# Kernel tuning notes

Measured on AMD Instinct MI355X. Metric: run time of the kernel, lower is better.

## Reference

```python
import jax, jax.numpy as jnp
import numpy as np

B, T, NH, HS = 2, 2048, 16, 64
C = NH * HS
V_SHIFT = 1          # value shift; queries start at position V_SHIFT
EXP_SCALE = 10.0     # exp_param_scale
KB_UP = 5.0          # kernel_beta_upbound


def setup_inputs() -> dict:
    key = jax.random.key(0)
    ks = jax.random.split(key, 8)
    s = 0.02
    return {
        "x": jax.random.normal(ks[0], (B, T, C), jnp.float32),
        # leaky-average key path: linear proj + per-head decay coefficient
        "W_la": jax.random.normal(ks[1], (C, C), jnp.float32) * s,
        "la_coef": jax.random.uniform(ks[2], (NH,), jnp.float32, 0.1, 0.9),
        "kernel_beta": jnp.ones((NH,), jnp.float32) / EXP_SCALE,
        "value_beta": jnp.ones((NH,), jnp.float32) * (-0.5) / EXP_SCALE,
        # value featurizer (lowrlinearconv): linear + per-head mixing coef
        "W_v": jax.random.normal(ks[3], (C, C), jnp.float32) * s,
        "v_coef": jax.random.uniform(ks[4], (NH,), jnp.float32, 0.0, 1.0),
        "W_proj": jax.random.normal(ks[5], (C, C), jnp.float32) * s,
    }


def reference(x, W_la, la_coef, kernel_beta, value_beta, W_v, v_coef, W_proj):
    B_, T_, C_ = x.shape
    # ---- keys: leaky average (per-head EMA recurrence) of linear projection ----
    xl = (x @ W_la).reshape(B_, T_, NH, HS)          # (B,T,nh,hs)
    alpha = la_coef.reshape(NH, 1)                   # per-head decay

    def step(carry, xt):  # carry,xt: (B,nh,hs)
        new = alpha * carry + (1.0 - alpha) * xt
        return new, new

    _, kt = jax.lax.scan(step, jnp.zeros((B_, NH, HS), x.dtype),
                         jnp.swapaxes(xl, 0, 1))    # (T,B,nh,hs)
    k = jnp.transpose(kt, (1, 2, 0, 3))              # (B,nh,T,hs)
    k = k / jnp.linalg.norm(k, axis=-1, keepdims=True)
    kb = jnp.exp(jnp.minimum(kernel_beta * EXP_SCALE, KB_UP)).reshape(1, NH, 1, 1)
    k = k * kb

    # ---- values: lowrlinearconv featurizer (shift=1, kernel=2) + L2 norm ----
    xv = (x @ W_v).reshape(B_, T_, NH, HS).transpose(0, 2, 1, 3)   # (B,nh,T,hs)
    xv_sh = jnp.concatenate([xv[:, :, 1:], jnp.zeros_like(xv[:, :, :1])], axis=2)
    c = v_coef.reshape(1, NH, 1, 1)
    v = xv_sh * (1.0 - c) + xv * c
    v = v / jnp.linalg.norm(v, axis=-1, keepdims=True)
    v = v * jnp.exp(value_beta * EXP_SCALE).reshape(1, NH, 1, 1)

    # ---- shifted-causal masked SDPA (scale=1); queries are positions >= V_SHIFT ----
    q = k[:, :, V_SHIFT:]                            # (B,nh,T-1,hs)
    scores = jnp.einsum('bhqd,bhkd->bhqk', q, k)
    qpos = jnp.arange(V_SHIFT, T_)[:, None]
    kpos = jnp.arange(T_)[None, :]
    mask = kpos < qpos                               # key j visible iff j < query position
    scores = jnp.where(mask, scores, -jnp.inf)
    att = jax.nn.softmax(scores, axis=-1)
    y_att = jnp.einsum('bhqk,bhkd->bhqd', att, v)
    y = jnp.concatenate([jnp.zeros((B_, NH, V_SHIFT, HS), x.dtype), y_att], axis=2)
    y = jnp.transpose(y, (0, 2, 1, 3)).reshape(B_, T_, C_)
    return y @ W_proj                                # dropouts are eval-mode identity
```

## Files before the change

### kernel.cpp

```cpp
#include <hip/hip_runtime.h>
#include <hip/hip_bf16.h>

#define B_  2
#define T_  2048
#define NH_ 16
#define HS_ 64
#define C_  1024
#define SCL_ 128
#define SCN_ (T_ / SCL_)
#define NT_  (T_ / 64)
#define TEL_ 4096

typedef __attribute__((ext_vector_type(8))) short bf16x8;
typedef __attribute__((ext_vector_type(4))) float f32x4;

__device__ inline int pack_bf16(float a, float b) {
  union { __hip_bfloat16 h; unsigned short u; } ua, ub;
  ua.h = __float2bfloat16(a);
  ub.h = __float2bfloat16(b);
  return (int)(((unsigned)ub.u << 16) | (unsigned)ua.u);
}

__device__ inline void gl_lds16(const __hip_bfloat16* g, __hip_bfloat16* l) {
  __builtin_amdgcn_global_load_lds(
      (const __attribute__((address_space(1))) unsigned int*)g,
      (__attribute__((address_space(3))) unsigned int*)l, 16, 0, 0);
}

__global__ __launch_bounds__(256) void prep1_kernel(const float* __restrict__ x,
                                                    const float* __restrict__ W_la,
                                                    const float* __restrict__ W_v,
                                                    const float* __restrict__ W_proj,
                                                    __hip_bfloat16* __restrict__ x16,
                                                    __hip_bfloat16* __restrict__ Wcat,
                                                    __hip_bfloat16* __restrict__ WprojT) {
  __shared__ __hip_bfloat16 tile[64][66];
  const int bid = (int)blockIdx.x;
  if (bid < 2048) {
    const int i = (bid * 256 + (int)threadIdx.x) * 8;
    const float4 a = *reinterpret_cast<const float4*>(x + i);
    const float4 b = *reinterpret_cast<const float4*>(x + i + 4);
    union { int s[4]; int4 v; } u;
    u.s[0] = pack_bf16(a.x, a.y);
    u.s[1] = pack_bf16(a.z, a.w);
    u.s[2] = pack_bf16(b.x, b.y);
    u.s[3] = pack_bf16(b.z, b.w);
    *reinterpret_cast<int4*>(x16 + i) = u.v;
    return;
  }
  const int id = bid - 2048;
  const int z = id >> 8;
  const int rem = id & 255;
  const int bx = rem & 15, by = rem >> 4;
  const float* W = (z == 0) ? W_la : (z == 1) ? W_v : W_proj;
  __hip_bfloat16* WT = (z == 2) ? WprojT : Wcat + (size_t)z * C_ * C_;
  const int w = threadIdx.x >> 6, l = threadIdx.x & 63;
  const int n0 = bx * 64, k0 = by * 64;
#pragma unroll
  for (int r = 0; r < 16; ++r) {
    const int k = k0 + w * 16 + r;
    tile[w * 16 + r][l] = __float2bfloat16(W[(size_t)k * C_ + n0 + l]);
  }
  __syncthreads();
#pragma unroll
  for (int r = 0; r < 16; ++r) {
    const int nn = w * 16 + r;
    WT[(size_t)(n0 + nn) * C_ + k0 + l] = tile[l][nn];
  }
}

__global__ __launch_bounds__(256) void gemm_in_kernel(const __hip_bfloat16* __restrict__ A,
                                                      const __hip_bfloat16* __restrict__ BT,
                                                      float* __restrict__ C0,
                                                      float* __restrict__ C1) {
  __shared__ __hip_bfloat16 As[2 * 128 * 32];
  __shared__ __hip_bfloat16 Bs[2 * 128 * 32];
  const int tid = threadIdx.x;
  const int m0 = blockIdx.y * 128, n0 = blockIdx.x * 128;
  const int w = tid >> 6, l = tid & 63;
  const int n = l & 15, kg = l >> 4;
  const int m0w = (w & 1) * 64, n0w = (w >> 1) * 64;

  const int r0 = tid >> 2, o0 = (tid & 3) * 8;
  const __hip_bfloat16* ag0 = A + (size_t)(m0 + r0) * C_ + o0;
  const __hip_bfloat16* ag1 = A + (size_t)(m0 + 64 + r0) * C_ + o0;
  const __hip_bfloat16* bg0 = BT + (size_t)(n0 + r0) * C_ + o0;
  const __hip_bfloat16* bg1 = BT + (size_t)(n0 + 64 + r0) * C_ + o0;

  f32x4 acc[4][4];
#pragma unroll
  for (int i = 0; i < 4; ++i)
#pragma unroll
    for (int j = 0; j < 4; ++j) acc[i][j] = f32x4{0.f, 0.f, 0.f, 0.f};

  auto stage = [&](int kk, int buf) {
    __hip_bfloat16* a = As + buf * 4096;
    __hip_bfloat16* b = Bs + buf * 4096;
    gl_lds16(ag0 + kk, a + tid * 8);
    gl_lds16(ag1 + kk, a + 2048 + tid * 8);
    gl_lds16(bg0 + kk, b + tid * 8);
    gl_lds16(bg1 + kk, b + 2048 + tid * 8);
  };

  stage(0, 0);
  int cur = 0;
  for (int k0 = 0; k0 < C_; k0 += 32) {
    asm volatile("" ::: "memory");
    __builtin_amdgcn_s_barrier();
    asm volatile("" ::: "memory");
    if (k0 + 32 < C_) {
      stage(k0 + 32, cur ^ 1);
      asm volatile("s_waitcnt vmcnt(4)" ::: "memory");
    } else {
      asm volatile("s_waitcnt vmcnt(0)" ::: "memory");
    }
    __builtin_amdgcn_s_barrier();
    asm volatile("" ::: "memory");

    const __hip_bfloat16* Ab = As + cur * 4096;
    const __hip_bfloat16* Bb = Bs + cur * 4096;
    bf16x8 af[4], bf[4];
#pragma unroll
    for (int ms = 0; ms < 4; ++ms)
      af[ms] = *reinterpret_cast<const bf16x8*>(Ab + (m0w + ms * 16 + n) * 32 + kg * 8);
#pragma unroll
    for (int ns = 0; ns < 4; ++ns)
      bf[ns] = *reinterpret_cast<const bf16x8*>(Bb + (n0w + ns * 16 + n) * 32 + kg * 8);
#pragma unroll
    for (int ms = 0; ms < 4; ++ms)
#pragma unroll
      for (int ns = 0; ns < 4; ++ns)
        acc[ms][ns] = __builtin_amdgcn_mfma_f32_16x16x32_bf16(af[ms], bf[ns], acc[ms][ns], 0, 0, 0);
    cur ^= 1;
  }

  float* Cb = (n0 < C_) ? C0 : C1;
  const int nc = (n0 < C_) ? n0 : n0 - C_;
#pragma unroll
  for (int ms = 0; ms < 4; ++ms) {
#pragma unroll
    for (int r = 0; r < 4; ++r) {
      const int row = m0 + m0w + ms * 16 + kg * 4 + r;
      float* cp = Cb + (size_t)row * C_ + nc + n0w + n;
#pragma unroll
      for (int ns = 0; ns < 4; ++ns) cp[ns * 16] = acc[ms][ns][r];
    }
  }
}

__global__ __launch_bounds__(256) void gemm_proj_kernel(const __hip_bfloat16* __restrict__ A,
                                                        const __hip_bfloat16* __restrict__ BT,
                                                        float* __restrict__ Cout) {
  __shared__ __hip_bfloat16 As[2 * 64 * 32];
  __shared__ __hip_bfloat16 Bs[2 * 128 * 32];
  const int tid = threadIdx.x;
  const int m0 = blockIdx.y * 64, n0 = blockIdx.x * 128;
  const int w = tid >> 6, l = tid & 63;
  const int n = l & 15, kg = l >> 4;

  const int r0 = tid >> 2, o0 = (tid & 3) * 8;
  const __hip_bfloat16* ag = A + (size_t)(m0 + r0) * C_ + o0;
  const __hip_bfloat16* bg0 = BT + (size_t)(n0 + r0) * C_ + o0;
  const __hip_bfloat16* bg1 = BT + (size_t)(n0 + 64 + r0) * C_ + o0;

  f32x4 acc[4][2];
#pragma unroll
  for (int i = 0; i < 4; ++i)
#pragma unroll
    for (int j = 0; j < 2; ++j) acc[i][j] = f32x4{0.f, 0.f, 0.f, 0.f};

  auto stage = [&](int kk, int buf) {
    __hip_bfloat16* a = As + buf * 2048;
    __hip_bfloat16* b = Bs + buf * 4096;
    gl_lds16(ag + kk, a + tid * 8);
    gl_lds16(bg0 + kk, b + tid * 8);
    gl_lds16(bg1 + kk, b + 2048 + tid * 8);
  };

  stage(0, 0);
  int cur = 0;
  for (int k0 = 0; k0 < C_; k0 += 32) {
    asm volatile("" ::: "memory");
    __builtin_amdgcn_s_barrier();
    asm volatile("" ::: "memory");
    if (k0 + 32 < C_) {
      stage(k0 + 32, cur ^ 1);
      asm volatile("s_waitcnt vmcnt(3)" ::: "memory");
    } else {
      asm volatile("s_waitcnt vmcnt(0)" ::: "memory");
    }
    __builtin_amdgcn_s_barrier();
    asm volatile("" ::: "memory");

    const __hip_bfloat16* Ab = As + cur * 2048;
    const __hip_bfloat16* Bb = Bs + cur * 4096;
    bf16x8 af[4], bf[2];
#pragma unroll
    for (int ms = 0; ms < 4; ++ms)
      af[ms] = *reinterpret_cast<const bf16x8*>(Ab + (ms * 16 + n) * 32 + kg * 8);
#pragma unroll
    for (int ns = 0; ns < 2; ++ns)
      bf[ns] = *reinterpret_cast<const bf16x8*>(Bb + (w * 32 + ns * 16 + n) * 32 + kg * 8);
#pragma unroll
    for (int ms = 0; ms < 4; ++ms)
#pragma unroll
      for (int ns = 0; ns < 2; ++ns)
        acc[ms][ns] = __builtin_amdgcn_mfma_f32_16x16x32_bf16(af[ms], bf[ns], acc[ms][ns], 0, 0, 0);
    cur ^= 1;
  }

#pragma unroll
  for (int ms = 0; ms < 4; ++ms) {
#pragma unroll
    for (int r = 0; r < 4; ++r) {
      const int row = m0 + ms * 16 + kg * 4 + r;
      float* cp = Cout + (size_t)row * C_ + n0 + w * 32 + n;
#pragma unroll
      for (int ns = 0; ns < 2; ++ns) cp[ns * 16] = acc[ms][ns][r];
    }
  }
}

__global__ __launch_bounds__(256) void prep2_kernel(const float* __restrict__ xv,
                                                    const float* __restrict__ xl,
                                                    __hip_bfloat16* __restrict__ vt,
                                                    float* __restrict__ loc,
                                                    float* __restrict__ carr,
                                                    const float* __restrict__ value_beta,
                                                    const float* __restrict__ v_coef,
                                                    const float* __restrict__ la_coef) {
  __shared__ float4 smem4[2048];
  const int bid = (int)blockIdx.x;
  if (bid < 1024) {
    __hip_bfloat16 (*tile)[66] = reinterpret_cast<__hip_bfloat16(*)[66]>(smem4);
    const int tc = bid % NT_;
    const int bh = bid / NT_;
    const int h = bh % NH_, b = bh / NH_;
    const int t0 = tc * 64;
    const int w = threadIdx.x >> 6, l = threadIdx.x & 63;

    const float c = v_coef[h];
    const float vb = expf(value_beta[h] * 10.0f);

    for (int r = 0; r < 16; ++r) {
      const int tl = w * 16 + r;
      const int t = t0 + tl;
      const float* base = xv + ((size_t)b * T_ + t) * C_ + h * HS_ + l;
      const float cu = base[0];
      const float nxt = (t + 1 < T_) ? base[C_] : 0.0f;
      float val = nxt * (1.0f - c) + cu * c;
      float ssum = val * val;
#pragma unroll
      for (int m = 32; m; m >>= 1) ssum += __shfl_xor(ssum, m);
      tile[tl][l] = __float2bfloat16(val * (vb / sqrtf(ssum)));
    }
    __syncthreads();
    __hip_bfloat16* vtb = vt + (size_t)(bh * NT_ + tc) * TEL_;
    const int kk = l >> 3, j = l & 7;
    for (int rr = 0; rr < 16; ++rr) {
      const int hs = w * 16 + rr;
      vtb[(kk * 64 + hs) * 8 + j] = tile[l][hs];
    }
    return;
  }
  {
    float* buf = reinterpret_cast<float*>(smem4);
    const int idx = bid - 1024;
    const int c = idx % SCN_;
    const int bh = idx / SCN_;
    const int b = bh / NH_, h = bh % NH_;
    const int tid = threadIdx.x;
    const int t0 = c * SCL_;

    const float alpha = la_coef[h];
    const float onema = 1.0f - alpha;
    const float4* src4 = reinterpret_cast<const float4*>(xl + (size_t)b * T_ * C_ + h * HS_);

    float4* buf4 = reinterpret_cast<float4*>(buf);
#pragma unroll
    for (int i = 0; i < (SCL_ * HS_ / 4) / 256; ++i) {
      const int ix = tid + i * 256;
      const int tt = ix >> 4, d4 = ix & 15;
      buf4[tt * 16 + d4] = src4[(size_t)(t0 + tt) * (C_ / 4) + d4];
    }
    __syncthreads();
    if (tid < 64) {
      const int d = tid;
      float c2 = 0.0f;
#pragma unroll 8
      for (int tt = 0; tt < SCL_; ++tt) {
        c2 = alpha * c2 + onema * buf[tt * HS_ + d];
        buf[tt * HS_ + d] = c2;
      }
      carr[(size_t)(bh * SCN_ + c) * HS_ + d] = c2;
    }
    __syncthreads();
    float4* dst4 = reinterpret_cast<float4*>(loc + ((size_t)bh * T_ + t0) * HS_);
#pragma unroll
    for (int i = 0; i < (SCL_ * HS_ / 4) / 256; ++i) dst4[tid + i * 256] = buf4[tid + i * 256];
  }
}

__global__ __launch_bounds__(256) void ema_fix_norm_kernel(const float* __restrict__ loc,
                                                           const float* __restrict__ carr,
                                                           __hip_bfloat16* __restrict__ kb16,
                                                           const float* __restrict__ la_coef,
                                                           const float* __restrict__ kernel_beta) {
  const int c = blockIdx.x % SCN_;
  const int bh = blockIdx.x / SCN_;
  const int h = bh % NH_;
  const int w = threadIdx.x >> 6, l = threadIdx.x & 63;

  const float alpha = la_coef[h];
  const float aL = __powf(alpha, (float)SCL_);
  const float kbs = expf(fminf(kernel_beta[h] * 10.0f, 5.0f));

  float A = 0.0f;
  for (int cc = 0; cc < c; ++cc) A = aL * A + carr[(size_t)(bh * SCN_ + cc) * HS_ + l];

  const float* lp = loc + ((size_t)bh * T_ + c * SCL_ + w * 32) * HS_ + l;
  __hip_bfloat16* kt = kb16 + (size_t)bh * NT_ * TEL_;
  const int g = l >> 3, j = l & 7;

  float s = __powf(alpha, (float)(w * 32 + 1));
  for (int rr = 0; rr < 32; ++rr) {
    const int t = c * SCL_ + w * 32 + rr;
    float val = lp[rr * HS_] + s * A;
    float ss = val * val;
#pragma unroll
    for (int m = 32; m; m >>= 1) ss += __shfl_xor(ss, m);
    const int tile = t >> 6, key = t & 63;
    kt[(size_t)tile * TEL_ + (g * 64 + key) * 8 + j] = __float2bfloat16(val * (kbs / sqrtf(ss)));
    s *= alpha;
  }
}

__global__ __launch_bounds__(256, 4) void attn_mfma_kernel(
    const __hip_bfloat16* __restrict__ kb,
    const __hip_bfloat16* __restrict__ vt,
    __hip_bfloat16* __restrict__ y) {
  __shared__ __hip_bfloat16 Ks[2][2 * TEL_];
  __shared__ __hip_bfloat16 Ps[4][16 * 64];

  const int id = (int)blockIdx.x;
  const int xcd = id & 7;
  const int s = id >> 3;
  const int bh = xcd + 8 * (s & 3);
  const int v = s >> 2;
  const int qt = (v < 16) ? (31 - v) : (v - 16);
  const int b = bh / NH_, h = bh % NH_;
  const int q0 = qt * 64;
  const int w = threadIdx.x >> 6;
  const int l = threadIdx.x & 63;
  const int n = l & 15;
  const int kg = l >> 4;
  const int qq = w * 16 + n;
  const int query = q0 + qq;
  const int lo = l * 8;
  const int tb = bh * NT_;
  const int so = w * 1024 + lo;

  bf16x8 qf0, qf1;
  {
    const __hip_bfloat16* qtile = kb + (size_t)(tb + qt) * TEL_;
    qf0 = *reinterpret_cast<const bf16x8*>(qtile + (kg * 64 + qq) * 8);
    qf1 = *reinterpret_cast<const bf16x8*>(qtile + ((kg + 4) * 64 + qq) * 8);
  }
  const __hip_bfloat16* vbase = vt + (size_t)tb * TEL_ + (kg * 64 + n) * 8;

  f32x4 accO[4];
#pragma unroll
  for (int i = 0; i < 4; ++i) accO[i] = f32x4{0.f, 0.f, 0.f, 0.f};
  float l_acc = 0.0f;

  __hip_bfloat16* Pw = Ps[w];
  int* Pwi = reinterpret_cast<int*>(Pw);

  auto stage2 = [&](int j0, int buf) {
    const size_t tg = (size_t)(tb + j0) * TEL_;
    __hip_bfloat16* Kb = &Ks[buf][0];
    gl_lds16(kb + tg + so, Kb + so);
    gl_lds16(kb + tg + so + 512, Kb + so + 512);
    gl_lds16(kb + tg + TEL_ + so, Kb + TEL_ + so);
    gl_lds16(kb + tg + TEL_ + so + 512, Kb + TEL_ + so + 512);
  };
  auto stage1 = [&](int j0, int buf) {
    const size_t tg = (size_t)(tb + j0) * TEL_;
    __hip_bfloat16* Kb = &Ks[buf][0];
    gl_lds16(kb + tg + so, Kb + so);
    gl_lds16(kb + tg + so + 512, Kb + so + 512);
  };
  auto loadV = [&](int jt, bf16x8 (&vf)[2][4]) {
    const __hip_bfloat16* vp = vbase + (size_t)jt * TEL_;
#pragma unroll
    for (int ks = 0; ks < 2; ++ks)
#pragma unroll
      for (int mo = 0; mo < 4; ++mo)
        vf[ks][mo] = *reinterpret_cast<const bf16x8*>(vp + ks * 2048 + mo * 128);
  };
  auto computeS = [&](const __hip_bfloat16* Kc, f32x4 (&accS)[4]) {
    __builtin_amdgcn_s_setprio(1);
#pragma unroll
    for (int ms = 0; ms < 4; ++ms) {
      bf16x8 a0 = *reinterpret_cast<const bf16x8*>(Kc + (kg * 64 + ms * 16 + n) * 8);
      bf16x8 a1 = *reinterpret_cast<const bf16x8*>(Kc + ((kg + 4) * 64 + ms * 16 + n) * 8);
      f32x4 z{0.f, 0.f, 0.f, 0.f};
      z = __builtin_amdgcn_mfma_f32_16x16x32_bf16(a0, qf0, z, 0, 0, 0);
      accS[ms] = __builtin_amdgcn_mfma_f32_16x16x32_bf16(a1, qf1, z, 0, 0, 0);
    }
    __builtin_amdgcn_s_setprio(0);
  };
  auto softmaxStore = [&](const f32x4 (&accS)[4], bool diag) {
    if (!diag) {
#pragma unroll
      for (int ms = 0; ms < 4; ++ms) {
        const float p0 = __expf(accS[ms][0]), p1 = __expf(accS[ms][1]);
        const float p2 = __expf(accS[ms][2]), p3 = __expf(accS[ms][3]);
        l_acc += p0 + p1 + p2 + p3;
        const int po = n * 32 + (((ms * 4 + kg) ^ n) << 1);
        int2 pw;
        pw.x = pack_bf16(p0, p1);
        pw.y = pack_bf16(p2, p3);
        *reinterpret_cast<int2*>(&Pwi[po]) = pw;
      }
    } else {
#pragma unroll
      for (int ms = 0; ms < 4; ++ms) {
        const int kbase = ms * 16 + kg * 4;
        float p[4];
#pragma unroll
        for (int r = 0; r < 4; ++r) {
          const float e = __expf(accS[ms][r]);
          p[r] = (kbase + r < qq) ? e : 0.0f;
          l_acc += p[r];
        }
        const int po = n * 32 + (((ms * 4 + kg) ^ n) << 1);
        int2 pw;
        pw.x = pack_bf16(p[0], p[1]);
        pw.y = pack_bf16(p[2], p[3]);
        *reinterpret_cast<int2*>(&Pwi[po]) = pw;
      }
    }
  };
  auto pv = [&](const bf16x8 (&vf)[2][4]) {
    __builtin_amdgcn_s_setprio(1);
#pragma unroll
    for (int ks = 0; ks < 2; ++ks) {
      union { ushort4 u[2]; bf16x8 vv; } pr;
      const int ga = (ks * 8 + kg * 2) ^ n;
      const __hip_bfloat16* pp = Pw + n * 64;
      pr.u[0] = *reinterpret_cast<const ushort4*>(pp + ga * 4);
      pr.u[1] = *reinterpret_cast<const ushort4*>(pp + (ga ^ 1) * 4);
#pragma unroll
      for (int mo = 0; mo < 4; ++mo)
        accO[mo] = __builtin_amdgcn_mfma_f32_16x16x32_bf16(vf[ks][mo], pr.vv, accO[mo], 0, 0, 0);
    }
    __builtin_amdgcn_s_setprio(0);
  };

  if (qt >= 1) stage2(0, 0); else stage1(0, 0);

  int cur = 0;
  int jp = 0;
  for (; jp + 1 <= qt; jp += 2) {
    asm volatile("" ::: "memory");
    __builtin_amdgcn_s_barrier();
    asm volatile("" ::: "memory");

    bf16x8 vfA[2][4];
    loadV(jp, vfA);
    asm volatile("" ::: "memory");

    const int nx = jp + 2;
    if (nx + 1 <= qt) {
      stage2(nx, cur ^ 1);
      asm volatile("s_waitcnt vmcnt(12)" ::: "memory");
    } else if (nx <= qt) {
      stage1(nx, cur ^ 1);
      asm volatile("s_waitcnt vmcnt(10)" ::: "memory");
    } else {
      asm volatile("s_waitcnt vmcnt(8)" ::: "memory");
    }
    __builtin_amdgcn_s_barrier();
    asm volatile("" ::: "memory");

    f32x4 accS[4];
    computeS(&Ks[cur][0], accS);
    softmaxStore(accS, false);
    pv(vfA);

    asm volatile("" ::: "memory");

    bf16x8 vfB[2][4];
    loadV(jp + 1, vfB);
    computeS(&Ks[cur][TEL_], accS);
    softmaxStore(accS, jp + 1 == qt);
    pv(vfB);

    cur ^= 1;
  }
  if (jp <= qt) {
    asm volatile("" ::: "memory");
    __builtin_amdgcn_s_barrier();
    asm volatile("" ::: "memory");
    bf16x8 vfA[2][4];
    loadV(jp, vfA);
    asm volatile("s_waitcnt vmcnt(8)" ::: "memory");
    __builtin_amdgcn_s_barrier();
    asm volatile("" ::: "memory");
    f32x4 accS[4];
    computeS(&Ks[cur][0], accS);
    softmaxStore(accS, true);
    pv(vfA);
  }

  l_acc += __shfl_xor(l_acc, 16);
  l_acc += __shfl_xor(l_acc, 32);
  const float inv = (query == 0) ? 0.0f : 1.0f / l_acc;
  __hip_bfloat16* yb = y + ((size_t)b * T_ + query) * C_ + h * HS_;
#pragma unroll
  for (int mo = 0; mo < 4; ++mo) {
    int2 pkd;
    pkd.x = pack_bf16(accO[mo][0] * inv, accO[mo][1] * inv);
    pkd.y = pack_bf16(accO[mo][2] * inv, accO[mo][3] * inv);
    *reinterpret_cast<int2*>(yb + mo * 16 + kg * 4) = pkd;
  }
}

extern "C" void kernel_launch(void* const* d_in, const int* in_sizes, int n_in,
                              void* d_out, int out_size, void* d_ws, size_t ws_size,
                              hipStream_t stream) {
  const float* x           = (const float*)d_in[0];
  const float* W_la        = (const float*)d_in[1];
  const float* la_coef     = (const float*)d_in[2];
  const float* kernel_beta = (const float*)d_in[3];
  const float* value_beta  = (const float*)d_in[4];
  const float* W_v         = (const float*)d_in[5];
  const float* v_coef      = (const float*)d_in[6];
  const float* W_proj      = (const float*)d_in[7];
  float* out = (float*)d_out;

  char* wsb = (char*)d_ws;
  const size_t MB = 1024u * 1024u;
  __hip_bfloat16* x16    = (__hip_bfloat16*)(wsb);
  __hip_bfloat16* Wcat   = (__hip_bfloat16*)(wsb + 8 * MB);
  __hip_bfloat16* WprojT = (__hip_bfloat16*)(wsb + 12 * MB);
  float* carr            = (float*)(wsb + 14 * MB);
  float* xl              = (float*)(wsb + 16 * MB);
  float* xv              = (float*)(wsb + 32 * MB);
  __hip_bfloat16* kb16   = (__hip_bfloat16*)(wsb + 48 * MB);
  __hip_bfloat16* vt16   = (__hip_bfloat16*)(wsb + 56 * MB);
  float* loc             = (float*)(wsb + 64 * MB);
  __hip_bfloat16* y16    = (__hip_bfloat16*)(wsb + 16 * MB);
  (void)ws_size; (void)in_sizes; (void)n_in; (void)out_size;

  const int M = B_ * T_;

  prep1_kernel<<<dim3(2048 + 768), dim3(256), 0, stream>>>(x, W_la, W_v, W_proj, x16, Wcat, WprojT);
  gemm_in_kernel<<<dim3(2 * C_ / 128, M / 128), dim3(256), 0, stream>>>(x16, Wcat, xl, xv);
  prep2_kernel<<<dim3(1024 + 512), dim3(256), 0, stream>>>(xv, xl, vt16, loc, carr,
                                                           value_beta, v_coef, la_coef);
  ema_fix_norm_kernel<<<dim3(B_ * NH_ * SCN_), dim3(256), 0, stream>>>(loc, carr, kb16, la_coef, kernel_beta);
  attn_mfma_kernel<<<dim3(8 * 128), dim3(256), 0, stream>>>(kb16, vt16, y16);
  gemm_proj_kernel<<<dim3(C_ / 128, M / 64), dim3(256), 0, stream>>>(y16, WprojT, out);
}
```

Before: 203.2 us.

## Process two query tiles per attention block to reuse K/V loads

Each attention workgroup now handles 128 queries (two 64-query tiles) instead of 64, so every staged K tile and loaded V fragment feeds two sets of MFMAs. The grid is halved, the query-tile ordering becomes a paired balanced schedule, and launch bounds drop to 2 waves per SIMD to fit the doubled accumulators and P buffers. This is meant to cut global/LDS traffic per FLOP, at the cost of lower occupancy and fewer blocks, which may hurt latency hiding and load balance.

```diff
diff --git a/kernel.cpp b/kernel.cpp
--- a/kernel.cpp
+++ b/kernel.cpp
@@ -335,46 +335,48 @@
   }
 }
 
-__global__ __launch_bounds__(256, 4) void attn_mfma_kernel(
+__global__ __launch_bounds__(256, 2) void attn_mfma_kernel(
     const __hip_bfloat16* __restrict__ kb,
     const __hip_bfloat16* __restrict__ vt,
     __hip_bfloat16* __restrict__ y) {
   __shared__ __hip_bfloat16 Ks[2][2 * TEL_];
-  __shared__ __hip_bfloat16 Ps[4][16 * 64];
+  __shared__ __hip_bfloat16 Ps[4][2][16 * 64];
 
   const int id = (int)blockIdx.x;
   const int xcd = id & 7;
   const int s = id >> 3;
   const int bh = xcd + 8 * (s & 3);
   const int v = s >> 2;
-  const int qt = (v < 16) ? (31 - v) : (v - 16);
+  const int u = (v < 8) ? v : (23 - v);
   const int b = bh / NH_, h = bh % NH_;
-  const int q0 = qt * 64;
+  const int q0 = u * 128;
   const int w = threadIdx.x >> 6;
   const int l = threadIdx.x & 63;
   const int n = l & 15;
   const int kg = l >> 4;
   const int qq = w * 16 + n;
-  const int query = q0 + qq;
   const int lo = l * 8;
   const int tb = bh * NT_;
   const int so = w * 1024 + lo;
 
-  bf16x8 qf0, qf1;
-  {
-    const __hip_bfloat16* qtile = kb + (size_t)(tb + qt) * TEL_;
-    qf0 = *reinterpret_cast<const bf16x8*>(qtile + (kg * 64 + qq) * 8);
-    qf1 = *reinterpret_cast<const bf16x8*>(qtile + ((kg + 4) * 64 + qq) * 8);
+  bf16x8 qf[2][2];
+#pragma unroll
+  for (int qg = 0; qg < 2; ++qg) {
+    const __hip_bfloat16* qtile = kb + (size_t)(tb + 2 * u + qg) * TEL_;
+    qf[qg][0] = *reinterpret_cast<const bf16x8*>(qtile + (kg * 64 + qq) * 8);
+    qf[qg][1] = *reinterpret_cast<const bf16x8*>(qtile + ((kg + 4) * 64 + qq) * 8);
   }
   const __hip_bfloat16* vbase = vt + (size_t)tb * TEL_ + (kg * 64 + n) * 8;
 
-  f32x4 accO[4];
-#pragma unroll
-  for (int i = 0; i < 4; ++i) accO[i] = f32x4{0.f, 0.f, 0.f, 0.f};
-  float l_acc = 0.0f;
-
-  __hip_bfloat16* Pw = Ps[w];
-  int* Pwi = reinterpret_cast<int*>(Pw);
+  f32x4 accO[2][4];
+#pragma unroll
+  for (int qg = 0; qg < 2; ++qg)
+#pragma unroll
+    for (int i = 0; i < 4; ++i) accO[qg][i] = f32x4{0.f, 0.f, 0.f, 0.f};
+  float l_acc[2] = {0.0f, 0.0f};
+
+  int* Pwi[2] = {reinterpret_cast<int*>(&Ps[w][0][0]),
+                 reinterpret_cast<int*>(&Ps[w][1][0])};
 
   auto stage2 = [&](int j0, int buf) {
     const size_t tg = (size_t)(tb + j0) * TEL_;
@@ -384,12 +386,6 @@
     gl_lds16(kb + tg + TEL_ + so, Kb + TEL_ + so);
     gl_lds16(kb + tg + TEL_ + so + 512, Kb + TEL_ + so + 512);
   };
-  auto stage1 = [&](int j0, int buf) {
-    const size_t tg = (size_t)(tb + j0) * TEL_;
-    __hip_bfloat16* Kb = &Ks[buf][0];
-    gl_lds16(kb + tg + so, Kb + so);
-    gl_lds16(kb + tg + so + 512, Kb + so + 512);
-  };
   auto loadV = [&](int jt, bf16x8 (&vf)[2][4]) {
     const __hip_bfloat16* vp = vbase + (size_t)jt * TEL_;
 #pragma unroll
@@ -398,30 +394,33 @@
       for (int mo = 0; mo < 4; ++mo)
         vf[ks][mo] = *reinterpret_cast<const bf16x8*>(vp + ks * 2048 + mo * 128);
   };
-  auto computeS = [&](const __hip_bfloat16* Kc, f32x4 (&accS)[4]) {
+  auto computeS2 = [&](const __hip_bfloat16* Kc, f32x4 (&aS)[2][4]) {
     __builtin_amdgcn_s_setprio(1);
 #pragma unroll
     for (int ms = 0; ms < 4; ++ms) {
       bf16x8 a0 = *reinterpret_cast<const bf16x8*>(Kc + (kg * 64 + ms * 16 + n) * 8);
       bf16x8 a1 = *reinterpret_cast<const bf16x8*>(Kc + ((kg + 4) * 64 + ms * 16 + n) * 8);
-      f32x4 z{0.f, 0.f, 0.f, 0.f};
-      z = __builtin_amdgcn_mfma_f32_16x16x32_bf16(a0, qf0, z, 0, 0, 0);
-      accS[ms] = __builtin_amdgcn_mfma_f32_16x16x32_bf16(a1, qf1, z, 0, 0, 0);
+#pragma unroll
+      for (int qg = 0; qg < 2; ++qg) {
+        f32x4 z{0.f, 0.f, 0.f, 0.f};
+        z = __builtin_amdgcn_mfma_f32_16x16x32_bf16(a0, qf[qg][0], z, 0, 0, 0);
+        aS[qg][ms] = __builtin_amdgcn_mfma_f32_16x16x32_bf16(a1, qf[qg][1], z, 0, 0, 0);
+      }
     }
     __builtin_amdgcn_s_setprio(0);
   };
-  auto softmaxStore = [&](const f32x4 (&accS)[4], bool diag) {
-    if (!diag) {
+  auto softmaxStore = [&](const f32x4 (&aS)[4], int qg, int dm) {
+    if (!dm) {
 #pragma unroll
       for (int ms = 0; ms < 4; ++ms) {
-        const float p0 = __expf(accS[ms][0]), p1 = __expf(accS[ms][1]);
-        const float p2 = __expf(accS[ms][2]), p3 = __expf(accS[ms][3]);
-        l_acc += p0 + p1 + p2 + p3;
+        const float p0 = __expf(aS[ms][0]), p1 = __expf(aS[ms][1]);
+        const float p2 = __expf(aS[ms][2]), p3 = __expf(aS[ms][3]);
+        l_acc[qg] += p0 + p1 + p2 + p3;
         const int po = n * 32 + (((ms * 4 + kg) ^ n) << 1);
         int2 pw;
         pw.x = pack_bf16(p0, p1);
         pw.y = pack_bf16(p2, p3);
-        *reinterpret_cast<int2*>(&Pwi[po]) = pw;
+        *reinterpret_cast<int2*>(&Pwi[qg][po]) = pw;
       }
     } else {
 #pragma unroll
@@ -430,100 +429,124 @@
         float p[4];
 #pragma unroll
         for (int r = 0; r < 4; ++r) {
-          const float e = __expf(accS[ms][r]);
+          const float e = __expf(aS[ms][r]);
           p[r] = (kbase + r < qq) ? e : 0.0f;
-          l_acc += p[r];
+          l_acc[qg] += p[r];
         }
         const int po = n * 32 + (((ms * 4 + kg) ^ n) << 1);
         int2 pw;
         pw.x = pack_bf16(p[0], p[1]);
         pw.y = pack_bf16(p[2], p[3]);
-        *reinterpret_cast<int2*>(&Pwi[po]) = pw;
+        *reinterpret_cast<int2*>(&Pwi[qg][po]) = pw;
       }
     }
   };
-  auto pv = [&](const bf16x8 (&vf)[2][4]) {
+  auto pv2 = [&](const bf16x8 (&vf)[2][4]) {
     __builtin_amdgcn_s_setprio(1);
 #pragma unroll
     for (int ks = 0; ks < 2; ++ks) {
-      union { ushort4 u[2]; bf16x8 vv; } pr;
       const int ga = (ks * 8 + kg * 2) ^ n;
-      const __hip_bfloat16* pp = Pw + n * 64;
-      pr.u[0] = *reinterpret_cast<const ushort4*>(pp + ga * 4);
-      pr.u[1] = *reinterpret_cast<const ushort4*>(pp + (ga ^ 1) * 4);
+      union { ushort4 uu[2]; bf16x8 vv; } pr[2];
+#pragma unroll
+      for (int qg = 0; qg < 2; ++qg) {
+        const __hip_bfloat16* pp = &Ps[w][qg][0] + n * 64;
+        pr[qg].uu[0] = *reinterpret_cast<const ushort4*>(pp + ga * 4);
+        pr[qg].uu[1] = *reinterpret_cast<const ushort4*>(pp + (ga ^ 1) * 4);
+      }
+#pragma unroll
+      for (int mo = 0; mo < 4; ++mo) {
+        accO[0][mo] = __builtin_amdgcn_mfma_f32_16x16x32_bf16(vf[ks][mo], pr[0].vv, accO[0][mo], 0, 0, 0);
+        accO[1][mo] = __builtin_amdgcn_mfma_f32_16x16x32_bf16(vf[ks][mo], pr[1].vv, accO[1][mo], 0, 0, 0);
+      }
+    }
+    __builtin_amdgcn_s_setprio(0);
+  };
+  auto pv1 = [&](const bf16x8 (&vf)[2][4]) {
+    __builtin_amdgcn_s_setprio(1);
+#pragma unroll
+    for (int ks = 0; ks < 2; ++ks) {
+      const int ga = (ks * 8 + kg * 2) ^ n;
+      union { ushort4 uu[2]; bf16x8 vv; } pr;
+      const __hip_bfloat16* pp = &Ps[w][1][0] + n * 64;
+      pr.uu[0] = *reinterpret_cast<const ushort4*>(pp + ga * 4);
+      pr.uu[1] = *reinterpret_cast<const ushort4*>(pp + (ga ^ 1) * 4);
 #pragma unroll
       for (int mo = 0; mo < 4; ++mo)
-        accO[mo] = __builtin_amdgcn_mfma_f32_16x16x32_bf16(vf[ks][mo], pr.vv, accO[mo], 0, 0, 0);
+        accO[1][mo] = __builtin_amdgcn_mfma_f32_16x16x32_bf16(vf[ks][mo], pr.vv, accO[1][mo], 0, 0, 0);
     }
     __builtin_amdgcn_s_setprio(0);
   };
 
-  if (qt >= 1) stage2(0, 0); else stage1(0, 0);
+  stage2(0, 0);
 
   int cur = 0;
-  int jp = 0;
-  for (; jp + 1 <= qt; jp += 2) {
+  for (int p = 0; p < u; ++p) {
     asm volatile("" ::: "memory");
     __builtin_amdgcn_s_barrier();
     asm volatile("" ::: "memory");
 
     bf16x8 vfA[2][4];
-    loadV(jp, vfA);
-    asm volatile("" ::: "memory");
-
-    const int nx = jp + 2;
-    if (nx + 1 <= qt) {
-      stage2(nx, cur ^ 1);
-      asm volatile("s_waitcnt vmcnt(12)" ::: "memory");
-    } else if (nx <= qt) {
-      stage1(nx, cur ^ 1);
-      asm volatile("s_waitcnt vmcnt(10)" ::: "memory");
-    } else {
-      asm volatile("s_waitcnt vmcnt(8)" ::: "memory");
-    }
-    __builtin_amdgcn_s_barrier();
-    asm volatile("" ::: "memory");
-
-    f32x4 accS[4];
-    computeS(&Ks[cur][0], accS);
-    softmaxStore(accS, false);
-    pv(vfA);
-
-    asm volatile("" ::: "memory");
+    loadV(2 * p, vfA);
+    asm volatile("" ::: "memory");
+    stage2(2 * p + 2, cur ^ 1);
+    asm volatile("s_waitcnt vmcnt(12)" ::: "memory");
+    __builtin_amdgcn_s_barrier();
+    asm volatile("" ::: "memory");
+
+    f32x4 aS[2][4];
+    computeS2(&Ks[cur][0], aS);
+    softmaxStore(aS[0], 0, 0);
+    softmaxStore(aS[1], 1, 0);
+    pv2(vfA);
 
     bf16x8 vfB[2][4];
-    loadV(jp + 1, vfB);
-    computeS(&Ks[cur][TEL_], accS);
-    softmaxStore(accS, jp + 1 == qt);
-    pv(vfB);
+    loadV(2 * p + 1, vfB);
+    computeS2(&Ks[cur][TEL_], aS);
+    softmaxStore(aS[0], 0, 0);
+    softmaxStore(aS[1], 1, 0);
+    pv2(vfB);
 
     cur ^= 1;
   }
-  if (jp <= qt) {
+
+  {
     asm volatile("" ::: "memory");
     __builtin_amdgcn_s_barrier();
     asm volatile("" ::: "memory");
     bf16x8 vfA[2][4];
-    loadV(jp, vfA);
+    loadV(2 * u, vfA);
     asm volatile("s_waitcnt vmcnt(8)" ::: "memory");
     __builtin_amdgcn_s_barrier();
     asm volatile("" ::: "memory");
-    f32x4 accS[4];
-    computeS(&Ks[cur][0], accS);
-    softmaxStore(accS, true);
-    pv(vfA);
-  }
-
-  l_acc += __shfl_xor(l_acc, 16);
-  l_acc += __shfl_xor(l_acc, 32);
-  const float inv = (query == 0) ? 0.0f : 1.0f / l_acc;
-  __hip_bfloat16* yb = y + ((size_t)b * T_ + query) * C_ + h * HS_;
-#pragma unroll
-  for (int mo = 0; mo < 4; ++mo) {
-    int2 pkd;
-    pkd.x = pack_bf16(accO[mo][0] * inv, accO[mo][1] * inv);
-    pkd.y = pack_bf16(accO[mo][2] * inv, accO[mo][3] * inv);
-    *reinterpret_cast<int2*>(yb + mo * 16 + kg * 4) = pkd;
+
+    f32x4 aS[2][4];
+    computeS2(&Ks[cur][0], aS);
+    softmaxStore(aS[0], 0, 1);
+    softmaxStore(aS[1], 1, 0);
+    pv2(vfA);
+
+    bf16x8 vfB[2][4];
+    loadV(2 * u + 1, vfB);
+    computeS2(&Ks[cur][TEL_], aS);
+    softmaxStore(aS[1], 1, 1);
+    pv1(vfB);
+  }
+
+#pragma unroll
+  for (int qg = 0; qg < 2; ++qg) {
+    float la = l_acc[qg];
+    la += __shfl_xor(la, 16);
+    la += __shfl_xor(la, 32);
+    const int query = q0 + qg * 64 + qq;
+    const float inv = (query == 0) ? 0.0f : 1.0f / la;
+    __hip_bfloat16* yb = y + ((size_t)b * T_ + query) * C_ + h * HS_;
+#pragma unroll
+    for (int mo = 0; mo < 4; ++mo) {
+      int2 pkd;
+      pkd.x = pack_bf16(accO[qg][mo][0] * inv, accO[qg][mo][1] * inv);
+      pkd.y = pack_bf16(accO[qg][mo][2] * inv, accO[qg][mo][3] * inv);
+      *reinterpret_cast<int2*>(yb + mo * 16 + kg * 4) = pkd;
+    }
   }
 }
 
@@ -561,6 +584,6 @@
   prep2_kernel<<<dim3(1024 + 512), dim3(256), 0, stream>>>(xv, xl, vt16, loc, carr,
                                                            value_beta, v_coef, la_coef);
   ema_fix_norm_kernel<<<dim3(B_ * NH_ * SCN_), dim3(256), 0, stream>>>(loc, carr, kb16, la_coef, kernel_beta);
-  attn_mfma_kernel<<<dim3(8 * 128), dim3(256), 0, stream>>>(kb16, vt16, y16);
+  attn_mfma_kernel<<<dim3(8 * 64), dim3(256), 0, stream>>>(kb16, vt16, y16);
   gemm_proj_kernel<<<dim3(C_ / 128, M / 64), dim3(256), 0, stream>>>(y16, WprojT, out);
 }
```

Measured after the change: 213.7 us. 1.05x slower.
